# Optimization experiments

Hardware: AMD Instinct MI355X
Metric: run time of the kernel (lower is better)

Reference implementation:

```python
import jax, jax.numpy as jnp
import numpy as np

B, T, D, H = 8, 1024, 1024, 16
HD = D // H
SCALE = HD ** -0.5


def setup_inputs() -> dict:
    key = jax.random.key(0)
    ks = jax.random.split(key, 12)
    s = 1.0 / np.sqrt(D)
    return {
        "query": jax.random.normal(ks[0], (B, T, D), jnp.float32),
        "key": jax.random.normal(ks[1], (B, T, D), jnp.float32),
        "value": jax.random.normal(ks[2], (B, T, D), jnp.float32),
        "stoichiometry": jax.random.uniform(ks[3], (B, T), jnp.float32),
        "key_padding_mask": jnp.zeros((B, T), jnp.bool_),
        "Wq": jax.random.uniform(ks[4], (D, D), jnp.float32, -s, s),
        "bq": jnp.zeros((D,), jnp.float32),
        "Wk": jax.random.uniform(ks[5], (D, D), jnp.float32, -s, s),
        "bk": jnp.zeros((D,), jnp.float32),
        "Wv": jax.random.uniform(ks[6], (D, D), jnp.float32, -s, s),
        "bv": jnp.zeros((D,), jnp.float32),
        "Wo": jax.random.uniform(ks[7], (D, D), jnp.float32, -s, s),
        "bo": jnp.zeros((D,), jnp.float32),
    }


def _split_heads(x):
    # [B,T,D] -> [B,H,T,HD]
    return x.reshape(B, T, H, HD).transpose(0, 2, 1, 3)


def reference(query, key, value, stoichiometry, key_padding_mask,
              Wq, bq, Wk, bk, Wv, bv, Wo, bo):
    # stoich_bias is None in this configuration, so stoichiometry is unused.
    Q = _split_heads(query @ Wq.T + bq)
    K = _split_heads(key @ Wk.T + bk)
    V = _split_heads(value @ Wv.T + bv)
    # [B,H,T,T] attention scores
    scores = jnp.einsum("bhtd,bhsd->bhts", Q, K) * SCALE
    scores = jnp.where(key_padding_mask[:, None, None, :], -jnp.inf, scores)
    probs = jax.nn.softmax(scores, axis=-1)  # dropout p=0 / eval mode
    out = jnp.einsum("bhts,bhsd->bhtd", probs, V)
    out = out.transpose(0, 2, 1, 3).reshape(B, T, D)
    return out @ Wo.T + bo
```

## Files before the change

kernel.cpp:

```cpp
#include <hip/hip_runtime.h>

#define BT   8192
#define DD   1024
#define TT   1024
#define NHD  64
#define CEXP 0.18033688011112042f

typedef unsigned short bf16_t;
typedef __attribute__((ext_vector_type(8))) short bf16x8;
typedef __attribute__((ext_vector_type(4))) float f32x4;

struct CvtArgs {
  const float* src[7];
  bf16_t*      dst[7];
  int          n8[7];
};

struct GemmArgs {
  const bf16_t* A[3];
  const bf16_t* Bw[3];
  const float*  bias[3];
  void*         C[3];
};

__device__ __forceinline__ unsigned short f2b(float f) {
  union { float f; unsigned u; } v; v.f = f;
  unsigned u = v.u;
  return (unsigned short)((u + 0x7FFFu + ((u >> 16) & 1u)) >> 16);
}

__device__ __forceinline__ unsigned cvt_pk(float lo, float hi) {
  unsigned r;
  asm("v_cvt_pk_bf16_f32 %0, %1, %2" : "=v"(r) : "v"(lo), "v"(hi));
  return r;
}

__device__ __forceinline__ float exp2_fast(float x) {
  float r;
  asm("v_exp_f32 %0, %1" : "=v"(r) : "v"(x));
  return r;
}

__device__ __forceinline__ void gload_lds16(const void* g, void* l) {
  __builtin_amdgcn_global_load_lds(
      (const __attribute__((address_space(1))) unsigned int*)g,
      (__attribute__((address_space(3))) unsigned int*)l, 16, 0, 0);
}

__global__ void cvt_kernel(CvtArgs a) {
  const int z = blockIdx.z;
  const float* __restrict__ s = a.src[z];
  bf16_t* __restrict__ d = a.dst[z];
  const int n8 = a.n8[z];
  for (int i = blockIdx.x * blockDim.x + threadIdx.x; i < n8;
       i += gridDim.x * blockDim.x) {
    const float4* sp = (const float4*)s + (size_t)i * 2;
    float4 x = sp[0], y = sp[1];
    union { unsigned short h[8]; uint4 v; } u;
    u.h[0] = f2b(x.x); u.h[1] = f2b(x.y); u.h[2] = f2b(x.z); u.h[3] = f2b(x.w);
    u.h[4] = f2b(y.x); u.h[5] = f2b(y.y); u.h[6] = f2b(y.z); u.h[7] = f2b(y.w);
    *((uint4*)(d + (size_t)i * 8)) = u.v;
  }
}

template<bool F32OUT>
__global__ __launch_bounds__(256, 2) void gemm_nt(GemmArgs g) {
  constexpr int K = DD, N = DD;
  const int z = blockIdx.z;
  const bf16_t* __restrict__ A  = g.A[z];
  const bf16_t* __restrict__ Bw = g.Bw[z];
  const float*  __restrict__ bias = g.bias[z];
  const int tid = threadIdx.x;
  const int lane = tid & 63, wid = tid >> 6;
  const int wr = wid >> 1, wc = wid & 1;
  const int brow = blockIdx.y * 128, bcol = blockIdx.x * 128;

  __shared__ bf16_t As[128 * 64];
  __shared__ bf16_t Bs[128 * 64];

  f32x4 acc[4][4];
#pragma unroll
  for (int m = 0; m < 4; ++m)
#pragma unroll
    for (int n = 0; n < 4; ++n) acc[m][n] = (f32x4){0.f, 0.f, 0.f, 0.f};

  const int srow = wid * 8 + (lane >> 3);
  const int sslot0 = lane & 7;

  auto stage = [&](int kt) {
    const int k0 = kt * 64;
#pragma unroll
    for (int q = 0; q < 4; ++q) {
      int r = q * 32 + srow;
      int sc = (sslot0 ^ (r & 7)) * 8;
      gload_lds16(A + (size_t)(brow + r) * K + k0 + sc,
                  (char*)As + q * 4096 + wid * 1024);
      gload_lds16(Bw + (size_t)(bcol + r) * K + k0 + sc,
                  (char*)Bs + q * 4096 + wid * 1024);
    }
  };

  stage(0);
  for (int kt = 0; kt < K / 64; ++kt) {
    __syncthreads();
#pragma unroll
    for (int ks = 0; ks < 2; ++ks) {
      bf16x8 af[4], bfr[4];
#pragma unroll
      for (int m = 0; m < 4; ++m) {
        int row = wr * 64 + m * 16 + (lane & 15);
        int slot = (ks * 4 + (lane >> 4)) ^ (row & 7);
        af[m] = *(const bf16x8*)((const char*)As + row * 128 + slot * 16);
      }
#pragma unroll
      for (int n = 0; n < 4; ++n) {
        int row = wc * 64 + n * 16 + (lane & 15);
        int slot = (ks * 4 + (lane >> 4)) ^ (row & 7);
        bfr[n] = *(const bf16x8*)((const char*)Bs + row * 128 + slot * 16);
      }
#pragma unroll
      for (int m = 0; m < 4; ++m)
#pragma unroll
        for (int n = 0; n < 4; ++n)
          acc[m][n] = __builtin_amdgcn_mfma_f32_16x16x32_bf16(af[m], bfr[n],
                                                              acc[m][n], 0, 0, 0);
    }
    __syncthreads();
    if (kt + 1 < K / 64) stage(kt + 1);
  }

  const int rl = (lane >> 4) * 4;
  const int cl = lane & 15;
#pragma unroll
  for (int n = 0; n < 4; ++n) {
    const int col = bcol + wc * 64 + n * 16 + cl;
    const float bv = bias[col];
#pragma unroll
    for (int m = 0; m < 4; ++m) {
      const int row0 = brow + wr * 64 + m * 16 + rl;
#pragma unroll
      for (int r = 0; r < 4; ++r) {
        float v = acc[m][n][r] + bv;
        if (F32OUT)
          ((float*)g.C[z])[(size_t)(row0 + r) * N + col] = v;
        else
          ((bf16_t*)g.C[z])[(size_t)(row0 + r) * N + col] = f2b(v);
      }
    }
  }
}

__global__ __launch_bounds__(256) void vt_kernel(const bf16_t* __restrict__ Vp,
                                                 bf16_t* __restrict__ Vt) {
  __shared__ bf16_t tile[64][72];
  const int bh = blockIdx.y, b = bh >> 4, h = bh & 15;
  const int t0 = blockIdx.x * 64;
  const int tid = threadIdx.x;
  const int r = tid >> 3, c8 = (tid & 7) * 8;
#pragma unroll
  for (int i = 0; i < 2; ++i) {
    int row = i * 32 + r;
    uint4 v = *(const uint4*)(Vp + (size_t)(b * TT + t0 + row) * DD + h * NHD + c8);
    *(uint4*)&tile[row][c8] = v;
  }
  __syncthreads();
#pragma unroll
  for (int i = 0; i < 2; ++i) {
    int d = i * 32 + r;
    union { bf16_t e[8]; uint4 v; } w;
#pragma unroll
    for (int j = 0; j < 8; ++j) w.e[j] = tile[c8 + j][d];
    *(uint4*)(Vt + ((size_t)bh * NHD + d) * TT + t0 + c8) = w.v;
  }
}

__global__ __launch_bounds__(256, 4) void attn_kernel(
    const bf16_t* __restrict__ Qg, const bf16_t* __restrict__ Kg,
    const bf16_t* __restrict__ VtG, bf16_t* __restrict__ Og) {
  const int qt = blockIdx.x;
  const int bh = blockIdx.y;
  const int b = bh >> 4, h = bh & 15;
  const int tid = threadIdx.x, lane = tid & 63, wid = tid >> 6;
  const int g = lane >> 4, q15 = lane & 15;
  const size_t baseQK = ((size_t)b * TT) * DD + (size_t)h * NHD;
  const size_t baseV  = (size_t)bh * NHD * TT;
  const int q0 = qt * 64;

  __shared__ bf16_t Qs[64 * 64];
  __shared__ bf16_t Ks[2][64 * 64];
  __shared__ bf16_t Vs[2][64 * 64];

  const int srow = wid * 8 + (lane >> 3);
  const int sslot0 = lane & 7;

#pragma unroll
  for (int q = 0; q < 2; ++q) {
    int r = q * 32 + srow;
    int sc = (sslot0 ^ (r & 7)) * 8;
    gload_lds16(Qg + baseQK + (size_t)(q0 + r) * DD + sc,
                (char*)Qs + q * 4096 + wid * 1024);
  }

  auto stageKV = [&](int kt, int buf) {
#pragma unroll
    for (int q = 0; q < 2; ++q) {
      int r = q * 32 + srow;
      int sc = (sslot0 ^ (r & 7)) * 8;
      gload_lds16(Kg + baseQK + (size_t)(kt * 64 + r) * DD + sc,
                  (char*)Ks[buf] + q * 4096 + wid * 1024);
      gload_lds16(VtG + baseV + (size_t)r * TT + kt * 64 + sc,
                  (char*)Vs[buf] + q * 4096 + wid * 1024);
    }
  };
  stageKV(0, 0);

  float mreg = -1e30f, lsum = 0.f;
  f32x4 o[4];
#pragma unroll
  for (int n = 0; n < 4; ++n) o[n] = (f32x4){0.f, 0.f, 0.f, 0.f};
  bf16x8 aq[2];

  const int shsrc0 = q15 + ((lane & 16) << 1);
  const bool up = (lane & 32) != 0;

  for (int kt = 0; kt < 16; ++kt) {
    __syncthreads();
    if (kt == 0) {
      int qrow = wid * 16 + q15;
#pragma unroll
      for (int ks = 0; ks < 2; ++ks) {
        int slot = (ks * 4 + g) ^ (qrow & 7);
        aq[ks] = *(const bf16x8*)((const char*)Qs + qrow * 128 + slot * 16);
      }
    }
    if (kt + 1 < 16) stageKV(kt + 1, (kt + 1) & 1);
    const char* K_ = (const char*)Ks[kt & 1];
    const char* V_ = (const char*)Vs[kt & 1];

    f32x4 s[4];
#pragma unroll
    for (int n = 0; n < 4; ++n) s[n] = (f32x4){0.f, 0.f, 0.f, 0.f};
#pragma unroll
    for (int ks = 0; ks < 2; ++ks) {
#pragma unroll
      for (int n = 0; n < 4; ++n) {
        int krow = n * 16 + q15;
        int slot = (ks * 4 + g) ^ (krow & 7);
        bf16x8 ak = *(const bf16x8*)(K_ + krow * 128 + slot * 16);
        s[n] = __builtin_amdgcn_mfma_f32_16x16x32_bf16(ak, aq[ks], s[n], 0, 0, 0);
      }
    }

    float vmax = s[0][0];
#pragma unroll
    for (int n = 0; n < 4; ++n)
#pragma unroll
      for (int r = 0; r < 4; ++r) vmax = fmaxf(vmax, s[n][r]);
    vmax = fmaxf(vmax, __shfl_xor(vmax, 16));
    vmax = fmaxf(vmax, __shfl_xor(vmax, 32));
    float nm = fmaxf(mreg, vmax);
    float bco = -nm * CEXP;
    float rs = 0.f;
#pragma unroll
    for (int n = 0; n < 4; ++n)
#pragma unroll
      for (int r = 0; r < 4; ++r) {
        s[n][r] = exp2_fast(s[n][r] * CEXP + bco);
        rs += s[n][r];
      }
    rs += __shfl_xor(rs, 16);
    rs += __shfl_xor(rs, 32);
    float fac = exp2_fast(mreg * CEXP + bco);
    mreg = nm;
    lsum = lsum * fac + rs;

    float frow[4];
#pragma unroll
    for (int r = 0; r < 4; ++r) frow[r] = __shfl(fac, g * 4 + r);
#pragma unroll
    for (int n = 0; n < 4; ++n)
#pragma unroll
      for (int r = 0; r < 4; ++r) o[n][r] *= frow[r];

    unsigned pk[4][2];
#pragma unroll
    for (int n = 0; n < 4; ++n) {
      pk[n][0] = cvt_pk(s[n][0], s[n][1]);
      pk[n][1] = cvt_pk(s[n][2], s[n][3]);
    }
    bf16x8 ap[2];
#pragma unroll
    for (int c = 0; c < 2; ++c) {
      unsigned lo0 = (unsigned)__shfl((int)pk[2 * c][0], shsrc0);
      unsigned lo1 = (unsigned)__shfl((int)pk[2 * c][1], shsrc0);
      unsigned lo2 = (unsigned)__shfl((int)pk[2 * c][0], shsrc0 + 16);
      unsigned lo3 = (unsigned)__shfl((int)pk[2 * c][1], shsrc0 + 16);
      unsigned hi0 = (unsigned)__shfl((int)pk[2 * c + 1][0], shsrc0);
      unsigned hi1 = (unsigned)__shfl((int)pk[2 * c + 1][1], shsrc0);
      unsigned hi2 = (unsigned)__shfl((int)pk[2 * c + 1][0], shsrc0 + 16);
      unsigned hi3 = (unsigned)__shfl((int)pk[2 * c + 1][1], shsrc0 + 16);
      union { unsigned u[4]; bf16x8 v; } t;
      t.u[0] = up ? hi0 : lo0;
      t.u[1] = up ? hi1 : lo1;
      t.u[2] = up ? hi2 : lo2;
      t.u[3] = up ? hi3 : lo3;
      ap[c] = t.v;
    }

#pragma unroll
    for (int c = 0; c < 2; ++c) {
#pragma unroll
      for (int nd = 0; nd < 4; ++nd) {
        int vrow = nd * 16 + q15;
        int slot = (c * 4 + g) ^ (vrow & 7);
        bf16x8 bv = *(const bf16x8*)(V_ + vrow * 128 + slot * 16);
        o[nd] = __builtin_amdgcn_mfma_f32_16x16x32_bf16(ap[c], bv, o[nd], 0, 0, 0);
      }
    }
  }

  float lrow[4];
#pragma unroll
  for (int r = 0; r < 4; ++r) lrow[r] = 1.f / __shfl(lsum, g * 4 + r);
#pragma unroll
  for (int nd = 0; nd < 4; ++nd)
#pragma unroll
    for (int r = 0; r < 4; ++r) {
      int row = q0 + wid * 16 + g * 4 + r;
      int col = nd * 16 + q15;
      Og[baseQK + (size_t)row * DD + col] = f2b(o[nd][r] * lrow[r]);
    }
}

extern "C" void kernel_launch(void* const* d_in, const int* in_sizes, int n_in,
                              void* d_out, int out_size, void* d_ws, size_t ws_size,
                              hipStream_t stream) {
  const float* q_in = (const float*)d_in[0];
  const float* k_in = (const float*)d_in[1];
  const float* v_in = (const float*)d_in[2];
  const float* Wq = (const float*)d_in[5];
  const float* bq = (const float*)d_in[6];
  const float* Wk = (const float*)d_in[7];
  const float* bk = (const float*)d_in[8];
  const float* Wv = (const float*)d_in[9];
  const float* bv = (const float*)d_in[10];
  const float* Wo = (const float*)d_in[11];
  const float* bo = (const float*)d_in[12];
  float* out = (float*)d_out;

  char* ws = (char*)d_ws;
  const size_t SZX = (size_t)BT * DD * 2;
  const size_t SZW = (size_t)DD * DD * 2;
  bf16_t* Xq  = (bf16_t*)(ws);
  bf16_t* Xk  = (bf16_t*)(ws + SZX);
  bf16_t* Xv  = (bf16_t*)(ws + 2 * SZX);
  bf16_t* Wqb = (bf16_t*)(ws + 3 * SZX);
  bf16_t* Wkb = (bf16_t*)(ws + 3 * SZX + SZW);
  bf16_t* Wvb = (bf16_t*)(ws + 3 * SZX + 2 * SZW);
  bf16_t* Wob = (bf16_t*)(ws + 3 * SZX + 3 * SZW);
  bf16_t* Qp  = (bf16_t*)(ws + 3 * SZX + 4 * SZW);
  bf16_t* Kp  = Qp + (size_t)BT * DD;
  bf16_t* Vp  = Kp + (size_t)BT * DD;
  bf16_t* attn = Xq;
  bf16_t* Vt   = Xk;

  CvtArgs ca;
  ca.src[0] = q_in; ca.dst[0] = Xq;  ca.n8[0] = BT * DD / 8;
  ca.src[1] = k_in; ca.dst[1] = Xk;  ca.n8[1] = BT * DD / 8;
  ca.src[2] = v_in; ca.dst[2] = Xv;  ca.n8[2] = BT * DD / 8;
  ca.src[3] = Wq;   ca.dst[3] = Wqb; ca.n8[3] = DD * DD / 8;
  ca.src[4] = Wk;   ca.dst[4] = Wkb; ca.n8[4] = DD * DD / 8;
  ca.src[5] = Wv;   ca.dst[5] = Wvb; ca.n8[5] = DD * DD / 8;
  ca.src[6] = Wo;   ca.dst[6] = Wob; ca.n8[6] = DD * DD / 8;
  cvt_kernel<<<dim3(512, 1, 7), 256, 0, stream>>>(ca);

  GemmArgs gp;
  gp.A[0] = Xq; gp.A[1] = Xk; gp.A[2] = Xv;
  gp.Bw[0] = Wqb; gp.Bw[1] = Wkb; gp.Bw[2] = Wvb;
  gp.bias[0] = bq; gp.bias[1] = bk; gp.bias[2] = bv;
  gp.C[0] = Qp; gp.C[1] = Kp; gp.C[2] = Vp;
  gemm_nt<false><<<dim3(DD / 128, BT / 128, 3), 256, 0, stream>>>(gp);

  vt_kernel<<<dim3(TT / 64, 128), 256, 0, stream>>>(Vp, Vt);

  attn_kernel<<<dim3(TT / 64, 128), 256, 0, stream>>>(Qp, Kp, Vt, attn);

  GemmArgs go;
  go.A[0] = attn; go.A[1] = attn; go.A[2] = attn;
  go.Bw[0] = Wob; go.Bw[1] = Wob; go.Bw[2] = Wob;
  go.bias[0] = bo; go.bias[1] = bo; go.bias[2] = bo;
  go.C[0] = out; go.C[1] = out; go.C[2] = out;
  gemm_nt<true><<<dim3(DD / 128, BT / 128, 1), 256, 0, stream>>>(go);
}
```

Measured before the change: 348.9 us.

## Rewrite GEMM with triple-buffered pipeline and attention with register-direct loads

The projection GEMM becomes a persistent-over-z kernel. It triple-buffers LDS with BK=32, manages vmcnt waits explicitly, raises MFMA issue priority, and remaps blocks for L2 locality. The attention kernel drops LDS staging and loads K and V fragments directly into registers. It also reorders the MFMA operands so row statistics need no shuffles, and applies lazy max rescaling (only when the running max grows by more than a threshold). The aim is to remove barrier and LDS round-trip overhead and improve overlap, at the cost of more register pressure and uncoalesced-ish global loads in attention.

After: 487.0 us. +39.6%, slower.

```diff
diff --git a/kernel.cpp b/kernel.cpp
--- a/kernel.cpp
+++ b/kernel.cpp
@@ -46,6 +46,9 @@
       (const __attribute__((address_space(1))) unsigned int*)g,
       (__attribute__((address_space(3))) unsigned int*)l, 16, 0, 0);
 }
+
+#define LGKM0() do { asm volatile("s_waitcnt lgkmcnt(0)" ::: "memory"); \
+                     __builtin_amdgcn_sched_barrier(0); } while (0)
 
 __global__ void cvt_kernel(CvtArgs a) {
   const int z = blockIdx.z;
@@ -63,90 +66,116 @@
   }
 }
 
-template<bool F32OUT>
-__global__ __launch_bounds__(256, 2) void gemm_nt(GemmArgs g) {
+template<bool F32OUT, int NZ>
+__global__ __launch_bounds__(256, 3) void gemm_pz(GemmArgs ga) {
+  __shared__ char lds[3 * 16384];
   constexpr int K = DD, N = DD;
-  const int z = blockIdx.z;
-  const bf16_t* __restrict__ A  = g.A[z];
-  const bf16_t* __restrict__ Bw = g.Bw[z];
-  const float*  __restrict__ bias = g.bias[z];
-  const int tid = threadIdx.x;
-  const int lane = tid & 63, wid = tid >> 6;
+  const int tid = threadIdx.x, lane = tid & 63, wid = tid >> 6;
   const int wr = wid >> 1, wc = wid & 1;
-  const int brow = blockIdx.y * 128, bcol = blockIdx.x * 128;
-
-  __shared__ bf16_t As[128 * 64];
-  __shared__ bf16_t Bs[128 * 64];
-
-  f32x4 acc[4][4];
-#pragma unroll
-  for (int m = 0; m < 4; ++m)
-#pragma unroll
-    for (int n = 0; n < 4; ++n) acc[m][n] = (f32x4){0.f, 0.f, 0.f, 0.f};
-
-  const int srow = wid * 8 + (lane >> 3);
-  const int sslot0 = lane & 7;
-
-  auto stage = [&](int kt) {
-    const int k0 = kt * 64;
-#pragma unroll
-    for (int q = 0; q < 4; ++q) {
-      int r = q * 32 + srow;
-      int sc = (sslot0 ^ (r & 7)) * 8;
-      gload_lds16(A + (size_t)(brow + r) * K + k0 + sc,
-                  (char*)As + q * 4096 + wid * 1024);
-      gload_lds16(Bw + (size_t)(bcol + r) * K + k0 + sc,
-                  (char*)Bs + q * 4096 + wid * 1024);
+  const int g4 = lane >> 4, q15 = lane & 15;
+  const int lin = blockIdx.x;
+  const int c8 = lin & 7, j = lin >> 3;
+  const int by = c8 * 8 + (j >> 3);
+  const int bx = j & 7;
+  const int brow = by * 128, bcol = bx * 128;
+
+  int osA[2], osB[2];
+#pragma unroll
+  for (int i = 0; i < 2; ++i) {
+    int idx = i * 256 + tid;
+    int sr = idx >> 3;
+    int sl = (idx & 7) ^ (sr & 7);
+    int r  = sr * 2 + (sl >> 2);
+    int k0 = (sl & 3) * 8;
+    osA[i] = (brow + r) * K + k0;
+    osB[i] = (bcol + r) * K + k0;
+  }
+
+  int offA[4], offB[4];
+#pragma unroll
+  for (int mm = 0; mm < 4; ++mm) {
+    int row = wr * 64 + mm * 16 + q15;
+    offA[mm] = (row >> 1) * 128 +
+               (((((row & 1) << 2) + g4) ^ ((row >> 1) & 7)) << 4);
+  }
+#pragma unroll
+  for (int nn = 0; nn < 4; ++nn) {
+    int row = wc * 64 + nn * 16 + q15;
+    offB[nn] = 8192 + (row >> 1) * 128 +
+               (((((row & 1) << 2) + g4) ^ ((row >> 1) & 7)) << 4);
+  }
+
+  for (int z = 0; z < NZ; ++z) {
+    const bf16_t* __restrict__ Az = ga.A[z];
+    const bf16_t* __restrict__ Bz = ga.Bw[z];
+
+    f32x4 acc[4][4];
+#pragma unroll
+    for (int m = 0; m < 4; ++m)
+#pragma unroll
+      for (int n = 0; n < 4; ++n) acc[m][n] = (f32x4){0.f, 0.f, 0.f, 0.f};
+
+    auto stageTile = [&](int kt, int bufo) {
+#pragma unroll
+      for (int i = 0; i < 2; ++i)
+        gload_lds16(Az + osA[i] + kt * 32,
+                    lds + bufo + i * 4096 + wid * 1024);
+#pragma unroll
+      for (int i = 0; i < 2; ++i)
+        gload_lds16(Bz + osB[i] + kt * 32,
+                    lds + bufo + 8192 + i * 4096 + wid * 1024);
+    };
+
+    stageTile(0, 0);
+    stageTile(1, 16384);
+    int rb = 0, sb = 32768;
+
+#pragma unroll 1
+    for (int kt = 0; kt < 32; ++kt) {
+      if (kt < 31) asm volatile("s_waitcnt vmcnt(4)" ::: "memory");
+      else         asm volatile("s_waitcnt vmcnt(0)" ::: "memory");
+      __builtin_amdgcn_s_barrier();
+      const char* bp = lds + rb;
+      bf16x8 af[4], bf[4];
+#pragma unroll
+      for (int mm = 0; mm < 4; ++mm) af[mm] = *(const bf16x8*)(bp + offA[mm]);
+#pragma unroll
+      for (int nn = 0; nn < 4; ++nn) bf[nn] = *(const bf16x8*)(bp + offB[nn]);
+      if (kt < 30) stageTile(kt + 2, sb);
+      LGKM0();
+      __builtin_amdgcn_s_setprio(1);
+#pragma unroll
+      for (int mm = 0; mm < 4; ++mm)
+#pragma unroll
+        for (int nn = 0; nn < 4; ++nn)
+          acc[mm][nn] = __builtin_amdgcn_mfma_f32_16x16x32_bf16(
+              af[mm], bf[nn], acc[mm][nn], 0, 0, 0);
+      __builtin_amdgcn_s_setprio(0);
+      rb = (rb == 32768) ? 0 : rb + 16384;
+      sb = (sb == 32768) ? 0 : sb + 16384;
     }
-  };
-
-  stage(0);
-  for (int kt = 0; kt < K / 64; ++kt) {
-    __syncthreads();
-#pragma unroll
-    for (int ks = 0; ks < 2; ++ks) {
-      bf16x8 af[4], bfr[4];
-#pragma unroll
-      for (int m = 0; m < 4; ++m) {
-        int row = wr * 64 + m * 16 + (lane & 15);
-        int slot = (ks * 4 + (lane >> 4)) ^ (row & 7);
-        af[m] = *(const bf16x8*)((const char*)As + row * 128 + slot * 16);
+
+    const float* __restrict__ bias = ga.bias[z];
+    float bv[4];
+#pragma unroll
+    for (int nn = 0; nn < 4; ++nn)
+      bv[nn] = bias[bcol + wc * 64 + nn * 16 + q15];
+#pragma unroll
+    for (int mm = 0; mm < 4; ++mm)
+#pragma unroll
+      for (int nn = 0; nn < 4; ++nn) {
+        const int col = bcol + wc * 64 + nn * 16 + q15;
+#pragma unroll
+        for (int r = 0; r < 4; ++r) {
+          const int row = brow + wr * 64 + mm * 16 + g4 * 4 + r;
+          float v = acc[mm][nn][r] + bv[nn];
+          if (F32OUT)
+            ((float*)ga.C[z])[(size_t)row * N + col] = v;
+          else
+            ((bf16_t*)ga.C[z])[(size_t)row * N + col] = f2b(v);
+        }
       }
-#pragma unroll
-      for (int n = 0; n < 4; ++n) {
-        int row = wc * 64 + n * 16 + (lane & 15);
-        int slot = (ks * 4 + (lane >> 4)) ^ (row & 7);
-        bfr[n] = *(const bf16x8*)((const char*)Bs + row * 128 + slot * 16);
-      }
-#pragma unroll
-      for (int m = 0; m < 4; ++m)
-#pragma unroll
-        for (int n = 0; n < 4; ++n)
-          acc[m][n] = __builtin_amdgcn_mfma_f32_16x16x32_bf16(af[m], bfr[n],
-                                                              acc[m][n], 0, 0, 0);
-    }
-    __syncthreads();
-    if (kt + 1 < K / 64) stage(kt + 1);
-  }
-
-  const int rl = (lane >> 4) * 4;
-  const int cl = lane & 15;
-#pragma unroll
-  for (int n = 0; n < 4; ++n) {
-    const int col = bcol + wc * 64 + n * 16 + cl;
-    const float bv = bias[col];
-#pragma unroll
-    for (int m = 0; m < 4; ++m) {
-      const int row0 = brow + wr * 64 + m * 16 + rl;
-#pragma unroll
-      for (int r = 0; r < 4; ++r) {
-        float v = acc[m][n][r] + bv;
-        if (F32OUT)
-          ((float*)g.C[z])[(size_t)(row0 + r) * N + col] = v;
-        else
-          ((bf16_t*)g.C[z])[(size_t)(row0 + r) * N + col] = f2b(v);
-      }
-    }
+    asm volatile("s_waitcnt vmcnt(0)" ::: "memory");
   }
 }
 
@@ -174,82 +203,62 @@
   }
 }
 
-__global__ __launch_bounds__(256, 4) void attn_kernel(
+__global__ __launch_bounds__(256, 3) void attn_kernel(
     const bf16_t* __restrict__ Qg, const bf16_t* __restrict__ Kg,
     const bf16_t* __restrict__ VtG, bf16_t* __restrict__ Og) {
-  const int qt = blockIdx.x;
-  const int bh = blockIdx.y;
+  const int lin = blockIdx.x;
+  const int qt = (lin >> 3) & 15;
+  const int bh = (lin & 7) | ((lin >> 7) << 3);
   const int b = bh >> 4, h = bh & 15;
   const int tid = threadIdx.x, lane = tid & 63, wid = tid >> 6;
   const int g = lane >> 4, q15 = lane & 15;
   const size_t baseQK = ((size_t)b * TT) * DD + (size_t)h * NHD;
   const size_t baseV  = (size_t)bh * NHD * TT;
-  const int q0 = qt * 64;
-
-  __shared__ bf16_t Qs[64 * 64];
-  __shared__ bf16_t Ks[2][64 * 64];
-  __shared__ bf16_t Vs[2][64 * 64];
-
-  const int srow = wid * 8 + (lane >> 3);
-  const int sslot0 = lane & 7;
-
-#pragma unroll
-  for (int q = 0; q < 2; ++q) {
-    int r = q * 32 + srow;
-    int sc = (sslot0 ^ (r & 7)) * 8;
-    gload_lds16(Qg + baseQK + (size_t)(q0 + r) * DD + sc,
-                (char*)Qs + q * 4096 + wid * 1024);
-  }
-
-  auto stageKV = [&](int kt, int buf) {
-#pragma unroll
-    for (int q = 0; q < 2; ++q) {
-      int r = q * 32 + srow;
-      int sc = (sslot0 ^ (r & 7)) * 8;
-      gload_lds16(Kg + baseQK + (size_t)(kt * 64 + r) * DD + sc,
-                  (char*)Ks[buf] + q * 4096 + wid * 1024);
-      gload_lds16(VtG + baseV + (size_t)r * TT + kt * 64 + sc,
-                  (char*)Vs[buf] + q * 4096 + wid * 1024);
-    }
+  const int qrow = qt * 64 + wid * 16 + q15;
+
+  bf16x8 aq[2];
+#pragma unroll
+  for (int ks = 0; ks < 2; ++ks)
+    aq[ks] = *(const bf16x8*)(Qg + baseQK + (size_t)qrow * DD + ks * 32 + g * 8);
+
+  bf16x8 kr[8];
+  auto loadK = [&](int kt) {
+#pragma unroll
+    for (int ks = 0; ks < 2; ++ks)
+#pragma unroll
+      for (int n = 0; n < 4; ++n)
+        kr[ks * 4 + n] = *(const bf16x8*)(
+            Kg + baseQK + (size_t)(kt * 64 + n * 16 + q15) * DD + ks * 32 + g * 8);
   };
-  stageKV(0, 0);
+  loadK(0);
 
   float mreg = -1e30f, lsum = 0.f;
   f32x4 o[4];
 #pragma unroll
   for (int n = 0; n < 4; ++n) o[n] = (f32x4){0.f, 0.f, 0.f, 0.f};
-  bf16x8 aq[2];
-
-  const int shsrc0 = q15 + ((lane & 16) << 1);
+
+  const int shsrcA = q15 + ((lane & 16) << 1);
   const bool up = (lane & 32) != 0;
 
   for (int kt = 0; kt < 16; ++kt) {
-    __syncthreads();
-    if (kt == 0) {
-      int qrow = wid * 16 + q15;
-#pragma unroll
-      for (int ks = 0; ks < 2; ++ks) {
-        int slot = (ks * 4 + g) ^ (qrow & 7);
-        aq[ks] = *(const bf16x8*)((const char*)Qs + qrow * 128 + slot * 16);
-      }
-    }
-    if (kt + 1 < 16) stageKV(kt + 1, (kt + 1) & 1);
-    const char* K_ = (const char*)Ks[kt & 1];
-    const char* V_ = (const char*)Vs[kt & 1];
+    bf16x8 vr[8];
+#pragma unroll
+    for (int nd = 0; nd < 4; ++nd)
+#pragma unroll
+      for (int c = 0; c < 2; ++c)
+        vr[nd * 2 + c] = *(const bf16x8*)(
+            VtG + baseV + (size_t)(nd * 16 + q15) * TT + kt * 64 + c * 32 + g * 8);
 
     f32x4 s[4];
 #pragma unroll
     for (int n = 0; n < 4; ++n) s[n] = (f32x4){0.f, 0.f, 0.f, 0.f};
 #pragma unroll
-    for (int ks = 0; ks < 2; ++ks) {
-#pragma unroll
-      for (int n = 0; n < 4; ++n) {
-        int krow = n * 16 + q15;
-        int slot = (ks * 4 + g) ^ (krow & 7);
-        bf16x8 ak = *(const bf16x8*)(K_ + krow * 128 + slot * 16);
-        s[n] = __builtin_amdgcn_mfma_f32_16x16x32_bf16(ak, aq[ks], s[n], 0, 0, 0);
-      }
-    }
+    for (int ks = 0; ks < 2; ++ks)
+#pragma unroll
+      for (int n = 0; n < 4; ++n)
+        s[n] = __builtin_amdgcn_mfma_f32_16x16x32_bf16(kr[ks * 4 + n], aq[ks],
+                                                       s[n], 0, 0, 0);
+    if (kt + 1 < 16) loadK(kt + 1);
 
     float vmax = s[0][0];
 #pragma unroll
@@ -258,8 +267,17 @@
       for (int r = 0; r < 4; ++r) vmax = fmaxf(vmax, s[n][r]);
     vmax = fmaxf(vmax, __shfl_xor(vmax, 16));
     vmax = fmaxf(vmax, __shfl_xor(vmax, 32));
-    float nm = fmaxf(mreg, vmax);
-    float bco = -nm * CEXP;
+    if (!__all(vmax <= mreg + 8.f)) {
+      float nm = fmaxf(mreg, vmax);
+      float fac = exp2_fast((mreg - nm) * CEXP);
+      mreg = nm;
+      lsum *= fac;
+#pragma unroll
+      for (int n = 0; n < 4; ++n)
+#pragma unroll
+        for (int r = 0; r < 4; ++r) o[n][r] *= fac;
+    }
+    float bco = -mreg * CEXP;
     float rs = 0.f;
 #pragma unroll
     for (int n = 0; n < 4; ++n)
@@ -270,17 +288,7 @@
       }
     rs += __shfl_xor(rs, 16);
     rs += __shfl_xor(rs, 32);
-    float fac = exp2_fast(mreg * CEXP + bco);
-    mreg = nm;
-    lsum = lsum * fac + rs;
-
-    float frow[4];
-#pragma unroll
-    for (int r = 0; r < 4; ++r) frow[r] = __shfl(fac, g * 4 + r);
-#pragma unroll
-    for (int n = 0; n < 4; ++n)
-#pragma unroll
-      for (int r = 0; r < 4; ++r) o[n][r] *= frow[r];
+    lsum += rs;
 
     unsigned pk[4][2];
 #pragma unroll
@@ -288,48 +296,41 @@
       pk[n][0] = cvt_pk(s[n][0], s[n][1]);
       pk[n][1] = cvt_pk(s[n][2], s[n][3]);
     }
-    bf16x8 ap[2];
+    bf16x8 bp[2];
 #pragma unroll
     for (int c = 0; c < 2; ++c) {
-      unsigned lo0 = (unsigned)__shfl((int)pk[2 * c][0], shsrc0);
-      unsigned lo1 = (unsigned)__shfl((int)pk[2 * c][1], shsrc0);
-      unsigned lo2 = (unsigned)__shfl((int)pk[2 * c][0], shsrc0 + 16);
-      unsigned lo3 = (unsigned)__shfl((int)pk[2 * c][1], shsrc0 + 16);
-      unsigned hi0 = (unsigned)__shfl((int)pk[2 * c + 1][0], shsrc0);
-      unsigned hi1 = (unsigned)__shfl((int)pk[2 * c + 1][1], shsrc0);
-      unsigned hi2 = (unsigned)__shfl((int)pk[2 * c + 1][0], shsrc0 + 16);
-      unsigned hi3 = (unsigned)__shfl((int)pk[2 * c + 1][1], shsrc0 + 16);
+      unsigned l0 = (unsigned)__shfl((int)pk[2 * c][0], shsrcA);
+      unsigned h0 = (unsigned)__shfl((int)pk[2 * c + 1][0], shsrcA);
+      unsigned l1 = (unsigned)__shfl((int)pk[2 * c][1], shsrcA);
+      unsigned h1 = (unsigned)__shfl((int)pk[2 * c + 1][1], shsrcA);
+      unsigned l2 = (unsigned)__shfl((int)pk[2 * c][0], shsrcA + 16);
+      unsigned h2 = (unsigned)__shfl((int)pk[2 * c + 1][0], shsrcA + 16);
+      unsigned l3 = (unsigned)__shfl((int)pk[2 * c][1], shsrcA + 16);
+      unsigned h3 = (unsigned)__shfl((int)pk[2 * c + 1][1], shsrcA + 16);
       union { unsigned u[4]; bf16x8 v; } t;
-      t.u[0] = up ? hi0 : lo0;
-      t.u[1] = up ? hi1 : lo1;
-      t.u[2] = up ? hi2 : lo2;
-      t.u[3] = up ? hi3 : lo3;
-      ap[c] = t.v;
+      t.u[0] = up ? h0 : l0;
+      t.u[1] = up ? h1 : l1;
+      t.u[2] = up ? h2 : l2;
+      t.u[3] = up ? h3 : l3;
+      bp[c] = t.v;
     }
 
 #pragma unroll
-    for (int c = 0; c < 2; ++c) {
-#pragma unroll
-      for (int nd = 0; nd < 4; ++nd) {
-        int vrow = nd * 16 + q15;
-        int slot = (c * 4 + g) ^ (vrow & 7);
-        bf16x8 bv = *(const bf16x8*)(V_ + vrow * 128 + slot * 16);
-        o[nd] = __builtin_amdgcn_mfma_f32_16x16x32_bf16(ap[c], bv, o[nd], 0, 0, 0);
-      }
-    }
-  }
-
-  float lrow[4];
-#pragma unroll
-  for (int r = 0; r < 4; ++r) lrow[r] = 1.f / __shfl(lsum, g * 4 + r);
-#pragma unroll
-  for (int nd = 0; nd < 4; ++nd)
-#pragma unroll
-    for (int r = 0; r < 4; ++r) {
-      int row = q0 + wid * 16 + g * 4 + r;
-      int col = nd * 16 + q15;
-      Og[baseQK + (size_t)row * DD + col] = f2b(o[nd][r] * lrow[r]);
-    }
+    for (int c = 0; c < 2; ++c)
+#pragma unroll
+      for (int nd = 0; nd < 4; ++nd)
+        o[nd] = __builtin_amdgcn_mfma_f32_16x16x32_bf16(vr[nd * 2 + c], bp[c],
+                                                        o[nd], 0, 0, 0);
+  }
+
+  const float inv = 1.f / lsum;
+#pragma unroll
+  for (int nd = 0; nd < 4; ++nd) {
+    union { unsigned u[2]; uint2 v; } w;
+    w.u[0] = cvt_pk(o[nd][0] * inv, o[nd][1] * inv);
+    w.u[1] = cvt_pk(o[nd][2] * inv, o[nd][3] * inv);
+    *(uint2*)(Og + baseQK + (size_t)qrow * DD + nd * 16 + g * 4) = w.v;
+  }
 }
 
 extern "C" void kernel_launch(void* const* d_in, const int* in_sizes, int n_in,
@@ -379,16 +380,16 @@
   gp.Bw[0] = Wqb; gp.Bw[1] = Wkb; gp.Bw[2] = Wvb;
   gp.bias[0] = bq; gp.bias[1] = bk; gp.bias[2] = bv;
   gp.C[0] = Qp; gp.C[1] = Kp; gp.C[2] = Vp;
-  gemm_nt<false><<<dim3(DD / 128, BT / 128, 3), 256, 0, stream>>>(gp);
+  gemm_pz<false, 3><<<512, 256, 0, stream>>>(gp);
 
   vt_kernel<<<dim3(TT / 64, 128), 256, 0, stream>>>(Vp, Vt);
 
-  attn_kernel<<<dim3(TT / 64, 128), 256, 0, stream>>>(Qp, Kp, Vt, attn);
+  attn_kernel<<<2048, 256, 0, stream>>>(Qp, Kp, Vt, attn);
 
   GemmArgs go;
   go.A[0] = attn; go.A[1] = attn; go.A[2] = attn;
   go.Bw[0] = Wob; go.Bw[1] = Wob; go.Bw[2] = Wob;
   go.bias[0] = bo; go.bias[1] = bo; go.bias[2] = bo;
   go.C[0] = out; go.C[1] = out; go.C[2] = out;
-  gemm_nt<true><<<dim3(DD / 128, BT / 128, 1), 256, 0, stream>>>(go);
-}
+  gemm_pz<true, 1><<<512, 256, 0, stream>>>(go);
+}
```
